# Optimization experiments

Measured on AMD Instinct MI355X. Metric: run time of the kernel, lower is better.

Reference implementation:

```python
import jax, jax.numpy as jnp
import numpy as np

K = 20
EPS = 1e-5

def _knn(x, k):
    # x: (B,C,N); returns indices of k nearest neighbors (incl. self): (B,N,k)
    xx = jnp.sum(x * x, axis=1)                          # (B,N)
    inner = jnp.einsum('bcn,bcm->bnm', x, x)             # (B,N,N)
    neg_d = 2.0 * inner - xx[:, :, None] - xx[:, None, :]
    return jax.lax.top_k(neg_d, k)[1]

def _graph_feature(x, k):
    # x: (B,C,N) -> (B,2C,N,k) with [x_j - x_i, x_i]
    idx = _knn(x, k)
    xt = jnp.transpose(x, (0, 2, 1))                     # (B,N,C)
    nb = jax.vmap(lambda f, i: f[i])(xt, idx)            # (B,N,k,C)
    ctr = xt[:, :, None, :]
    feat = jnp.concatenate([nb - ctr, jnp.broadcast_to(ctr, nb.shape)], axis=-1)
    return jnp.transpose(feat, (0, 3, 1, 2))

def _edge_block(h, w, g, b, k):
    # EdgeConv: graph feature -> 1x1 conv -> BN(eval, mean0/var1) -> LeakyReLU(0.2) -> max over k
    f = _graph_feature(h, k)
    f = jnp.einsum('oc,bcnk->bonk', w, f)
    f = g[None, :, None, None] * f / np.sqrt(1.0 + EPS) + b[None, :, None, None]
    f = jnp.where(f >= 0, f, 0.2 * f)
    return jnp.max(f, axis=-1)                           # (B,O,N)

def _forward(features_1, features_2, sw1, sg1, sb1, fw1, fg1, fb1, sw2, sg2, sb2, fw2, fg2, fb2, sw3, sg3, sb3, fw3, fg3, fb3, ew, eg, eb, att_w, tn_w, tn_wb, tn_bias, fc1_w, fc1_b, sc_w, sc_b):
    def dgcnn_pass(x):
        xyz = x[:, :3, :]
        sem = x[:, 3:, :]
        x1 = _edge_block(xyz, sw1, sg1, sb1, K)
        x2 = _edge_block(x1, sw2, sg2, sb2, K)
        x3 = _edge_block(x2, sw3, sg3, sb3, K)
        s1 = _edge_block(sem, fw1, fg1, fb1, K)
        s2 = _edge_block(s1, fw2, fg2, fb2, K)
        s3 = _edge_block(s2, fw3, fg3, fb3, K)
        h = jnp.concatenate([x3, s3], axis=1)            # (B,2*F3,N)
        h = jnp.einsum('oc,bcn->bon', ew, h)
        h = eg[None, :, None] * h / np.sqrt(1.0 + EPS) + eb[None, :, None]
        h = jnp.where(h >= 0, h, 0.2 * h)
        return jnp.transpose(h, (0, 2, 1))               # (B,N,F3)

    def attention(emb):
        gc = jnp.tanh(jnp.mean(jnp.einsum('bnf,fg->bng', emb, att_w), axis=1))  # (B,F)
        sc = jax.nn.sigmoid(jnp.einsum('bnf,bf->bn', emb, gc))[:, :, None]      # (B,N,1)
        pooled = jnp.einsum('bnf,bnk->bfk', emb, sc)                            # (B,F,1)
        return pooled, sc

    a1 = dgcnn_pass(features_1)
    a2 = dgcnn_pass(features_2)
    p1, att1 = attention(a1)
    p2, att2 = attention(a2)
    e1 = p1[:, :, 0]
    e2 = p2[:, :, 0]
    # NTN: e1^T W[:,:,t] e2 + V [e1;e2] + b
    scoring = jnp.einsum('bf,fgt,bg->bt', e1, tn_w, e2)
    block = jnp.einsum('tc,bc->bt', tn_wb, jnp.concatenate([e1, e2], axis=1))
    tscores = jax.nn.relu(scoring + block + tn_bias[:, 0][None, :])             # (B,T)
    h = jax.nn.relu(tscores @ fc1_w.T + fc1_b)
    score = jax.nn.sigmoid(h @ sc_w.T + sc_b).reshape(-1)                       # (B,)
    return score, att1, att2


def setup_inputs() -> dict:
    key = jax.random.key(0)
    ks = iter(jax.random.split(key, 40))
    def rn(shape, s=0.05):
        return jax.random.normal(next(ks), shape, dtype=jnp.float32) * s
    F1, F2, F3, T, BN = 64, 64, 128, 16, 16
    d = {}
    d['features_1'] = jax.random.normal(next(ks), (8, 131, 1024), dtype=jnp.float32)
    d['features_2'] = jax.random.normal(next(ks), (8, 131, 1024), dtype=jnp.float32)
    d['sw1'] = rn((F1, 6));        d['sg1'] = jnp.ones((F1,));  d['sb1'] = jnp.zeros((F1,))
    d['fw1'] = rn((F1, 256));      d['fg1'] = jnp.ones((F1,));  d['fb1'] = jnp.zeros((F1,))
    d['sw2'] = rn((F2, 2 * F1));   d['sg2'] = jnp.ones((F2,));  d['sb2'] = jnp.zeros((F2,))
    d['fw2'] = rn((F2, 2 * F1));   d['fg2'] = jnp.ones((F2,));  d['fb2'] = jnp.zeros((F2,))
    d['sw3'] = rn((F3, 2 * F2));   d['sg3'] = jnp.ones((F3,));  d['sb3'] = jnp.zeros((F3,))
    d['fw3'] = rn((F3, 2 * F2));   d['fg3'] = jnp.ones((F3,));  d['fb3'] = jnp.zeros((F3,))
    d['ew']  = rn((F3, 2 * F3));   d['eg']  = jnp.ones((F3,));  d['eb']  = jnp.zeros((F3,))
    d['att_w'] = rn((F3, F3))
    d['tn_w'] = rn((F3, F3, T))
    d['tn_wb'] = rn((T, 2 * F3))
    d['tn_bias'] = rn((T, 1))
    d['fc1_w'] = rn((BN, T));  d['fc1_b'] = jnp.zeros((BN,))
    d['sc_w'] = rn((1, BN));   d['sc_b'] = jnp.zeros((1,))
    return d


def reference(features_1, features_2, sw1, sg1, sb1, fw1, fg1, fb1, sw2, sg2, sb2, fw2, fg2, fb2, sw3, sg3, sb3, fw3, fg3, fb3, ew, eg, eb, att_w, tn_w, tn_wb, tn_bias, fc1_w, fc1_b, sc_w, sc_b):
    return _forward(features_1, features_2, sw1, sg1, sb1, fw1, fg1, fb1, sw2, sg2, sb2, fw2, fg2, fb2, sw3, sg3, sb3, fw3, fg3, fb3, ew, eg, eb, att_w, tn_w, tn_wb, tn_bias, fc1_w, fc1_b, sc_w, sc_b)
```

## Files before the change

kernel.cpp:

```cpp
#include <hip/hip_runtime.h>
#include <math.h>

#define INV_SQRT1P 0.99999500003749968754f

typedef short v8s  __attribute__((ext_vector_type(8)));
typedef float v16f __attribute__((ext_vector_type(16)));

static __device__ __forceinline__ float lrelu(float f){ return f >= 0.0f ? f : 0.2f*f; }

static __device__ __forceinline__ int lanecnt_below(unsigned long long m){
  int c = __builtin_amdgcn_mbcnt_lo((unsigned)m, 0u);
  return __builtin_amdgcn_mbcnt_hi((unsigned)(m >> 32), c);
}

__global__ void k_extract(const float* __restrict__ f, float* __restrict__ out, int c0, int Cout, int boff){
  int i = blockIdx.x*256 + threadIdx.x;
  int total = 8*Cout*1024;
  if (i >= total) return;
  int n  = i & 1023;
  int bc = i >> 10;
  int c  = bc % Cout;
  int b  = bc / Cout;
  out[((size_t)(((b+boff)<<10)+n))*Cout + c] = f[((size_t)(b*131 + c0 + c) << 10) + n];
}

__global__ __launch_bounds__(256) void k_pw(const float* __restrict__ X,
    unsigned short* __restrict__ PH, unsigned short* __restrict__ PL,
    float* __restrict__ xxout, const float* __restrict__ Wm,
    unsigned short* __restrict__ PWH, unsigned short* __restrict__ PWL,
    int C, int Kp, int O, int nwblk){
  int nkc = Kp >> 4;
  if ((int)blockIdx.x < nwblk){
    int gid = blockIdx.x*256 + threadIdx.x;
    int nchunk = (2*O/32)*nkc;
    if (gid >= nchunk*64) return;
    int lane = gid & 63;
    int chunk = gid >> 6;
    int jb = chunk / nkc, kc = chunk - jb*nkc;
    int j = jb*32 + (lane & 31);
    int k0 = kc*16 + ((lane>>5)<<3);
    unsigned short h[8], lo[8];
    #pragma unroll
    for (int t=0;t<8;t++){
      int k = k0 + t;
      float x = 0.f;
      if (k < C) x = (j < O) ? Wm[(size_t)j*2*C + k] : Wm[(size_t)(j-O)*2*C + C + k];
      unsigned u = __float_as_uint(x);
      unsigned h16 = (u + 0x7fffu + ((u>>16)&1u)) >> 16;
      float hf = __uint_as_float(h16 << 16);
      float lf = x - hf;
      unsigned ul = __float_as_uint(lf);
      unsigned l16 = (ul + 0x7fffu + ((ul>>16)&1u)) >> 16;
      h[t] = (unsigned short)h16; lo[t] = (unsigned short)l16;
    }
    size_t o = (size_t)chunk*512 + lane*8;
    *(v8s*)(PWH + o) = *(v8s*)h;
    *(v8s*)(PWL + o) = *(v8s*)lo;
  } else {
    int gid = (blockIdx.x - nwblk)*256 + threadIdx.x;
    int lane = gid & 63;
    int chunk = gid >> 6;
    int rb = chunk / nkc, kc = chunk - rb*nkc;
    int row = rb*32 + (lane & 31);
    int k0 = kc*16 + ((lane>>5)<<3);
    unsigned short h[8], lo[8];
    const float* Xr = X + (size_t)row*C;
    #pragma unroll
    for (int j=0;j<8;j++){
      int k = k0 + j;
      float x = (k < C) ? Xr[k] : 0.f;
      unsigned u = __float_as_uint(x);
      unsigned h16 = (u + 0x7fffu + ((u>>16)&1u)) >> 16;
      float hf = __uint_as_float(h16 << 16);
      float lf = x - hf;
      unsigned ul = __float_as_uint(lf);
      unsigned l16 = (ul + 0x7fffu + ((ul>>16)&1u)) >> 16;
      h[j] = (unsigned short)h16; lo[j] = (unsigned short)l16;
    }
    size_t o = (size_t)chunk*512 + lane*8;
    *(v8s*)(PH + o) = *(v8s*)h;
    *(v8s*)(PL + o) = *(v8s*)lo;
    if (kc == 0 && (lane & 32) == 0){
      float s = 0.f;
      for (int c=0;c<C;c++) s += Xr[c]*Xr[c];
      xxout[row] = s;
    }
  }
}

__global__ __launch_bounds__(512) void k_dy(const unsigned short* __restrict__ PH,
    const unsigned short* __restrict__ PL, const unsigned short* __restrict__ PWH,
    const unsigned short* __restrict__ PWL, const float* __restrict__ xx,
    int* __restrict__ idx, float* __restrict__ Y, int Kp, int N, int npair, int nymf){
  __shared__ float Sl[16][1024];
  int wave = threadIdx.x >> 6;
  int l = threadIdx.x & 63;
  int nkc = Kp >> 4;

  if ((int)blockIdx.x < nymf){
    int gw = blockIdx.x*8 + wave;
    int mt = gw / npair;
    int pair = gw - mt*npair;
    int jb0 = pair*2, jb1 = pair*2 + 1;
    size_t ao  = ((size_t)mt*nkc)*512 + l*8;
    size_t b0o = ((size_t)jb0*nkc)*512 + l*8;
    size_t b1o = ((size_t)jb1*nkc)*512 + l*8;
    v16f acc0, acc1;
    #pragma unroll
    for (int i=0;i<16;i++){ acc0[i] = 0.f; acc1[i] = 0.f; }
    for (int kc=0; kc<nkc; kc++){
      v8s Ah  = *(const v8s*)(PH + ao);
      v8s Al  = *(const v8s*)(PL + ao);
      v8s B0h = *(const v8s*)(PWH + b0o);
      v8s B0l = *(const v8s*)(PWL + b0o);
      v8s B1h = *(const v8s*)(PWH + b1o);
      v8s B1l = *(const v8s*)(PWL + b1o);
      acc0 = __builtin_amdgcn_mfma_f32_32x32x16_bf16(Ah, B0h, acc0, 0, 0, 0);
      acc1 = __builtin_amdgcn_mfma_f32_32x32x16_bf16(Ah, B1h, acc1, 0, 0, 0);
      acc0 = __builtin_amdgcn_mfma_f32_32x32x16_bf16(Ah, B0l, acc0, 0, 0, 0);
      acc1 = __builtin_amdgcn_mfma_f32_32x32x16_bf16(Ah, B1l, acc1, 0, 0, 0);
      acc0 = __builtin_amdgcn_mfma_f32_32x32x16_bf16(Al, B0h, acc0, 0, 0, 0);
      acc1 = __builtin_amdgcn_mfma_f32_32x32x16_bf16(Al, B1h, acc1, 0, 0, 0);
      ao += 512; b0o += 512; b1o += 512;
    }
    int rbase = mt*32;
    int c0 = pair*64 + (l & 31), c1 = c0 + 32;
    #pragma unroll
    for (int r=0;r<16;r++){
      int rl_ = (r&3) + ((r>>2)<<3) + ((l>>5)<<2);
      float* dst = Y + (size_t)(rbase + rl_)*N;
      dst[c0] = acc0[r];
      dst[c1] = acc1[r];
    }
    return;
  }

  int rb = blockIdx.x - nymf;
  int batch = rb >> 5;
  const float* xxb = xx + (batch<<10);
  int rbase_local = (rb & 31)*32;

  v16f acc[4];
  #pragma unroll
  for (int i=0;i<4;i++){
    #pragma unroll
    for (int j=0;j<16;j++) acc[i][j] = 0.f;
  }
  #pragma unroll
  for (int pp=0; pp<2; pp++){
    int pair = wave*2 + pp;
    size_t a   = ((size_t)rb*nkc)*512 + l*8;
    size_t b0o = ((size_t)(batch*32 + 2*pair)*nkc)*512 + l*8;
    size_t b1o = b0o + (size_t)nkc*512;
    for (int kc=0; kc<nkc; kc++){
      v8s Ah  = *(const v8s*)(PH + a);
      v8s Al  = *(const v8s*)(PL + a);
      v8s B0h = *(const v8s*)(PH + b0o);
      v8s B0l = *(const v8s*)(PL + b0o);
      v8s B1h = *(const v8s*)(PH + b1o);
      v8s B1l = *(const v8s*)(PL + b1o);
      acc[2*pp]   = __builtin_amdgcn_mfma_f32_32x32x16_bf16(Ah, B0h, acc[2*pp],   0, 0, 0);
      acc[2*pp+1] = __builtin_amdgcn_mfma_f32_32x32x16_bf16(Ah, B1h, acc[2*pp+1], 0, 0, 0);
      acc[2*pp]   = __builtin_amdgcn_mfma_f32_32x32x16_bf16(Ah, B0l, acc[2*pp],   0, 0, 0);
      acc[2*pp+1] = __builtin_amdgcn_mfma_f32_32x32x16_bf16(Ah, B1l, acc[2*pp+1], 0, 0, 0);
      acc[2*pp]   = __builtin_amdgcn_mfma_f32_32x32x16_bf16(Al, B0h, acc[2*pp],   0, 0, 0);
      acc[2*pp+1] = __builtin_amdgcn_mfma_f32_32x32x16_bf16(Al, B1h, acc[2*pp+1], 0, 0, 0);
      a += 512; b0o += 512; b1o += 512;
    }
  }

  #pragma unroll
  for (int h=0; h<2; h++){
    #pragma unroll
    for (int pp=0; pp<2; pp++){
      int pair = wave*2 + pp;
      int c0 = pair*64 + (l & 31), c1 = c0 + 32;
      float xc0 = xxb[c0], xc1 = xxb[c1];
      #pragma unroll
      for (int r = 0; r < 8; r++){
        int rr = h*8 + r;
        int rl = (rr&3) + (((rr>>2)&1)<<3) + ((l>>5)<<2);
        float xr = xxb[rbase_local + h*16 + rl];
        Sl[rl][c0] = 2.f*acc[2*pp][rr]   - xr - xc0;
        Sl[rl][c1] = 2.f*acc[2*pp+1][rr] - xr - xc1;
      }
    }
    __syncthreads();
    {
      int hi = l >> 5;
      int li = l & 31;
      int rloc = wave*2 + hi;
      int grow = rb*32 + h*16 + rloc;
      int out_base = grow*20;
      unsigned long long hm = hi ? 0xFFFFFFFF00000000ull : 0x00000000FFFFFFFFull;

      unsigned kv[32];
      #pragma unroll
      for (int j=0;j<32;j++){
        unsigned u = __float_as_uint(Sl[rloc][li + 32*j]);
        kv[j] = (u & 0x80000000u) ? ~u : (u | 0x80000000u);
      }

      unsigned lmax = kv[0];
      #pragma unroll
      for (int j=1;j<32;j++) lmax = lmax > kv[j] ? lmax : kv[j];

      unsigned tau = 0u;
      #pragma unroll
      for (int bit=31; bit>=0; --bit){
        unsigned cand = tau | (1u << bit);
        unsigned long long M = __ballot(lmax >= cand);
        int c = hi ? __popc((unsigned)(M >> 32)) : __popc((unsigned)M);
        tau = (c >= 20) ? cand : tau;
      }

      unsigned long long* sl = (unsigned long long*)&Sl[rloc][0];
      sl[li] = 0ull; sl[li+32] = 0ull;
      int b2 = 0;
      #pragma unroll
      for (int j=0;j<32;j++){
        bool p = kv[j] >= tau;
        unsigned long long M = __ballot(p) & hm;
        if (p){
          int s = b2 + lanecnt_below(M);
          if (s < 64) sl[s] = ((unsigned long long)kv[j] << 32) | (unsigned)(li + 32*j);
        }
        b2 += __popcll(M);
      }

      if (b2 <= 64){
        unsigned long long pk0 = sl[li], pk1 = sl[li+32];
        unsigned vcur = 0u;
        #pragma unroll
        for (int bit=31; bit>=0; --bit){
          unsigned long long cc = (unsigned long long)(vcur | (1u << bit)) << 32;
          unsigned long long B0 = __ballot(pk0 >= cc);
          unsigned long long B1 = __ballot(pk1 >= cc);
          int clo = __popc((unsigned)B0) + __popc((unsigned)B1);
          int chi = __popc((unsigned)(B0>>32)) + __popc((unsigned)(B1>>32));
          int c = hi ? chi : clo;
          vcur = (c >= 20) ? (vcur | (1u << bit)) : vcur;
        }
        unsigned k0 = (unsigned)(pk0 >> 32), k1 = (unsigned)(pk1 >> 32);
        unsigned long long G0 = __ballot(k0 > vcur) & hm;
        unsigned long long G1 = __ballot(k1 > vcur) & hm;
        int ng0 = __popcll(G0);
        int c1  = ng0 + __popcll(G1);
        if (k0 > vcur) idx[out_base + lanecnt_below(G0)] = (int)(pk0 & 0xffffffffu);
        if (k1 > vcur) idx[out_base + ng0 + lanecnt_below(G1)] = (int)(pk1 & 0xffffffffu);
        unsigned long long E0 = __ballot(k0 == vcur) & hm;
        unsigned long long E1 = __ballot(k1 == vcur) & hm;
        int ne0 = __popcll(E0);
        if (k0 == vcur){ int s = c1 + lanecnt_below(E0); if (s < 20) idx[out_base + s] = (int)(pk0 & 0xffffffffu); }
        if (k1 == vcur){ int s = c1 + ne0 + lanecnt_below(E1); if (s < 20) idx[out_base + s] = (int)(pk1 & 0xffffffffu); }
      } else {
        unsigned cur = 0u;
        #pragma unroll 1
        for (int bit=31; bit>=0; --bit){
          unsigned cand = cur | (1u << bit);
          int lc = 0;
          #pragma unroll
          for (int j=0;j<32;j++) lc += (kv[j] >= cand) ? 1 : 0;
          #pragma unroll
          for (int off=1; off<32; off<<=1) lc += __shfl_xor(lc, off, 64);
          cur = (lc >= 20) ? cand : cur;
        }
        int bse = 0;
        #pragma unroll 1
        for (int j=0;j<32;j++){
          unsigned long long Mg = __ballot(kv[j] > cur) & hm;
          if (kv[j] > cur){ int s = bse + lanecnt_below(Mg); idx[out_base + s] = li + 32*j; }
          bse += __popcll(Mg);
        }
        #pragma unroll 1
        for (int j=0;j<32;j++){
          unsigned long long Me = __ballot(kv[j] == cur) & hm;
          if (kv[j] == cur){ int s = bse + lanecnt_below(Me); if (s < 20) idx[out_base + s] = li + 32*j; }
          bse += __popcll(Me);
          if (bse >= 20) break;
        }
      }
    }
    __syncthreads();
  }
}

__global__ __launch_bounds__(256) void k_gthin(
    const float* __restrict__ Am, const float* __restrict__ Bm, float* __restrict__ Om,
    int K, int ldo, int wmode, const float* __restrict__ p1, const float* __restrict__ p2, int ep)
{
  __shared__ float As[64][33];
  __shared__ float Bs[64][68];
  int tid = threadIdx.x;
  int tx = tid & 15, ty = tid >> 4;
  int rbase = blockIdx.y*32, cbase = blockIdx.x*64;
  float acc[2][4];
  #pragma unroll
  for (int i=0;i<2;i++){ acc[i][0]=0.f; acc[i][1]=0.f; acc[i][2]=0.f; acc[i][3]=0.f; }

  for (int c0=0; c0<K; c0+=64){
    int cw = K - c0; if (cw > 64) cw = 64;
    #pragma unroll
    for (int p=0; p<2; p++){
      int idx = p*256 + tid;
      int kq = idx & 15, row = idx >> 4;
      const float* src = Am + (size_t)(rbase+row)*K + c0 + kq*4;
      float4 v = {0.f,0.f,0.f,0.f};
      if (kq*4 + 4 <= cw) v = *(const float4*)src;
      else {
        if (kq*4+0 < cw) v.x = src[0];
        if (kq*4+1 < cw) v.y = src[1];
        if (kq*4+2 < cw) v.z = src[2];
        if (kq*4+3 < cw) v.w = src[3];
      }
      As[kq*4+0][row]=v.x; As[kq*4+1][row]=v.y; As[kq*4+2][row]=v.z; As[kq*4+3][row]=v.w;
    }
    #pragma unroll
    for (int p=0; p<4; p++){
      int idx = p*256 + tid;
      int kq = idx & 15, col = idx >> 4;
      int j = cbase + col;
      const float* src = (wmode > 0)
          ? ((j < wmode) ? Bm + (size_t)j*2*K + c0 + kq*4
                         : Bm + (size_t)(j-wmode)*2*K + K + c0 + kq*4)
          : Bm + (size_t)j*K + c0 + kq*4;
      float4 v = {0.f,0.f,0.f,0.f};
      if (kq*4 + 4 <= cw) v = *(const float4*)src;
      else {
        if (kq*4+0 < cw) v.x = src[0];
        if (kq*4+1 < cw) v.y = src[1];
        if (kq*4+2 < cw) v.z = src[2];
        if (kq*4+3 < cw) v.w = src[3];
      }
      int swb = (kq & 14) << 1;
      int cs = col ^ swb;
      Bs[kq*4+0][cs]=v.x; Bs[kq*4+1][cs]=v.y; Bs[kq*4+2][cs]=v.z; Bs[kq*4+3][cs]=v.w;
    }
    __syncthreads();
    for (int k=0;k<cw;k++){
      int sw = ((k>>3)&7)<<2;
      float a0 = As[k][ty*2], a1 = As[k][ty*2+1];
      float b[4];
      *(float4*)b = *(const float4*)&Bs[k][(tx*4) ^ sw];
      acc[0][0]+=a0*b[0]; acc[0][1]+=a0*b[1]; acc[0][2]+=a0*b[2]; acc[0][3]+=a0*b[3];
      acc[1][0]+=a1*b[0]; acc[1][1]+=a1*b[1]; acc[1][2]+=a1*b[2]; acc[1][3]+=a1*b[3];
    }
    __syncthreads();
  }
  #pragma unroll
  for (int i=0;i<2;i++){
    int r = rbase + ty*2 + i;
    float o[4];
    #pragma unroll
    for (int j=0;j<4;j++){
      int cc = cbase + tx*4 + j;
      float v = acc[i][j];
      if (ep == 1) v = lrelu(p1[cc]*v*INV_SQRT1P + p2[cc]);
      o[j] = v;
    }
    *(float4*)(Om + (size_t)r*ldo + cbase + tx*4) = *(float4*)o;
  }
}

__global__ __launch_bounds__(256) void k_edge(const float* __restrict__ Y, const int* __restrict__ idx,
    const float* __restrict__ g, const float* __restrict__ bias,
    float* __restrict__ out, int O, int ldo, int ooff){
  int rpb = 256/O;
  int rloc = threadIdx.x/O;
  int o = threadIdx.x - rloc*O;
  int row = blockIdx.x*rpb + rloc;
  int b = row >> 10;
  __shared__ int js[4][20];
  int nj = rpb*20;
  if (threadIdx.x < nj) js[threadIdx.x/20][threadIdx.x%20] = idx[(blockIdx.x*rpb)*20 + threadIdx.x];
  __syncthreads();
  int O2 = O*2;
  float y1c = Y[(size_t)row*O2 + o];
  float d   = Y[(size_t)row*O2 + O + o] - y1c;
  float sc  = g[o] * INV_SQRT1P;
  float bb  = bias[o];
  const float* Yb = Y + ((size_t)(b<<10))*O2;
  float best = -1e38f;
  #pragma unroll
  for (int k=0;k<20;k++){
    float f = sc * (Yb[(size_t)js[rloc][k]*O2 + o] + d) + bb;
    best = fmaxf(best, lrelu(f));
  }
  out[(size_t)row*ldo + ooff + o] = best;
}

__global__ __launch_bounds__(1024) void k_meangc(const float* __restrict__ emb,
     const float* __restrict__ att_w, float* __restrict__ gc){
  int b = blockIdx.x; int f = threadIdx.x & 127; int ny = threadIdx.x >> 7;
  const float* e = emb + ((size_t)(b<<10) + ny*128)*128 + f;
  float s = 0.f;
  for (int n=0;n<128;n++) s += e[n*128];
  __shared__ float red[8][128];
  __shared__ float mr[128];
  red[ny][f] = s;
  __syncthreads();
  if (ny == 0){
    float t = 0.f;
    #pragma unroll
    for (int i=0;i<8;i++) t += red[i][f];
    mr[f] = t * (1.0f/1024.0f);
  }
  __syncthreads();
  if (threadIdx.x < 128){
    int g = threadIdx.x;
    float s2 = 0.f;
    for (int ff=0; ff<128; ff++) s2 += mr[ff]*att_w[ff*128+g];
    gc[b*128+g] = tanhf(s2);
  }
}

__global__ __launch_bounds__(64) void k_sc(const float* __restrict__ emb, const float* __restrict__ gc,
     float* __restrict__ sc, float* __restrict__ attout){
  int row = blockIdx.x; int l = threadIdx.x; int b = row >> 10;
  const float* e  = emb + (size_t)row*128;
  const float* gb = gc + b*128;
  float p = e[l]*gb[l] + e[l+64]*gb[l+64];
  #pragma unroll
  for (int off=32; off>0; off>>=1) p += __shfl_xor(p, off, 64);
  if (l == 0){
    float s = 1.0f/(1.0f + expf(-p));
    sc[row] = s;
    attout[row] = s;
  }
}

__global__ __launch_bounds__(1024) void k_pool(const float* __restrict__ emb, const float* __restrict__ sc,
     float* __restrict__ ep){
  int b = blockIdx.x; int f = threadIdx.x & 127; int ny = threadIdx.x >> 7;
  const float* e  = emb + ((size_t)(b<<10) + ny*128)*128 + f;
  const float* sb = sc + (b<<10) + ny*128;
  float s = 0.f;
  for (int n=0;n<128;n++) s += e[n*128]*sb[n];
  __shared__ float red[8][128];
  red[ny][f] = s;
  __syncthreads();
  if (ny == 0){
    float t = 0.f;
    #pragma unroll
    for (int i=0;i<8;i++) t += red[i][f];
    ep[b*128+f] = t;
  }
}

__global__ __launch_bounds__(256) void k_tnet(const float* __restrict__ e1, const float* __restrict__ e2,
    const float* __restrict__ tn_w, const float* __restrict__ tn_wb, const float* __restrict__ tn_bias,
    float* __restrict__ tsout){
  int b = blockIdx.x; int t = threadIdx.x; int tt = t & 15; int fs = t >> 4;
  __shared__ float E1[128], E2[128], red[16][17];
  if (t < 128){ E1[t] = e1[b*128+t]; E2[t] = e2[b*128+t]; }
  __syncthreads();
  float acc = 0.f;
  for (int f = fs*8; f < fs*8+8; f++){
    const float* tw = tn_w + f*128*16 + tt;
    float partial = 0.f;
    for (int g=0; g<128; g++) partial += E2[g]*tw[g*16];
    acc += E1[f]*partial;
  }
  red[fs][tt] = acc;
  __syncthreads();
  if (t < 16){
    float s = 0.f;
    #pragma unroll
    for (int i=0;i<16;i++) s += red[i][t];
    float acc2 = 0.f;
    for (int c=0;c<128;c++) acc2 += tn_wb[t*256+c]*E1[c] + tn_wb[t*256+128+c]*E2[c];
    float v = s + acc2 + tn_bias[t];
    tsout[b*16+t] = v > 0.f ? v : 0.f;
  }
}

__global__ __launch_bounds__(128) void k_score2(const float* __restrict__ ts,
   const float* __restrict__ fc1_w, const float* __restrict__ fc1_b,
   const float* __restrict__ sc_w, const float* __restrict__ sc_b, float* __restrict__ out){
  int t = threadIdx.x; int b = t >> 4, i = t & 15;
  __shared__ float h2[8][17];
  float a = 0.f;
  #pragma unroll
  for (int k=0;k<16;k++) a += ts[b*16+k]*fc1_w[i*16+k];
  a += fc1_b[i];
  h2[b][i] = a > 0.f ? a : 0.f;
  __syncthreads();
  if (t < 8){
    float s = 0.f;
    #pragma unroll
    for (int k=0;k<16;k++) s += h2[t][k]*sc_w[k];
    s += sc_b[0];
    out[t] = 1.0f/(1.0f + expf(-s));
  }
}

extern "C" void kernel_launch(void* const* d_in, const int* in_sizes, int n_in,
                              void* d_out, int out_size, void* d_ws, size_t ws_size,
                              hipStream_t stream){
  const float* f1  = (const float*)d_in[0];
  const float* f2  = (const float*)d_in[1];
  const float* sw1 = (const float*)d_in[2];  const float* sg1 = (const float*)d_in[3];  const float* sb1 = (const float*)d_in[4];
  const float* fw1 = (const float*)d_in[5];  const float* fg1 = (const float*)d_in[6];  const float* fb1 = (const float*)d_in[7];
  const float* sw2 = (const float*)d_in[8];  const float* sg2 = (const float*)d_in[9];  const float* sb2 = (const float*)d_in[10];
  const float* fw2 = (const float*)d_in[11]; const float* fg2 = (const float*)d_in[12]; const float* fb2 = (const float*)d_in[13];
  const float* sw3 = (const float*)d_in[14]; const float* sg3 = (const float*)d_in[15]; const float* sb3 = (const float*)d_in[16];
  const float* fw3 = (const float*)d_in[17]; const float* fg3 = (const float*)d_in[18]; const float* fb3 = (const float*)d_in[19];
  const float* ew  = (const float*)d_in[20]; const float* eg  = (const float*)d_in[21]; const float* eb  = (const float*)d_in[22];
  const float* att_w   = (const float*)d_in[23];
  const float* tn_w    = (const float*)d_in[24];
  const float* tn_wb   = (const float*)d_in[25];
  const float* tn_bias = (const float*)d_in[26];
  const float* fc1_w   = (const float*)d_in[27];
  const float* fc1_b   = (const float*)d_in[28];
  const float* sc_w    = (const float*)d_in[29];
  const float* sc_b    = (const float*)d_in[30];

  float* W    = (float*)d_ws;
  float* T0   = W;
  float* T1   = W + 2097152;
  float* X3S3 = W + 4194304;
  float* EMB  = W + 8388608;
  float* xx   = W + 10485760;
  float* gcb  = W + 10504192;
  float* scb  = W + 10506240;
  float* ep   = W + 10522624;
  float* tsb  = W + 10524672;
  int*   idxb = (int*)(W + 10524800);
  unsigned short* PH = (unsigned short*)(W + 10852480);
  unsigned short* PL = (unsigned short*)(W + 11901056);
  unsigned short* PWH = (unsigned short*)(W + 12949632);
  unsigned short* PWL = (unsigned short*)(W + 12966016);
  float* REG  = W + 12982400;

  (void)ws_size;
  float* out = (float*)d_out;

  auto edge = [&](const float* xin, int C, int O,
                  const float* w, const float* g, const float* bb,
                  float* xout, int ldo, int ooff){
    int Kp = (C + 15) & ~15;
    int nkc = Kp >> 4;
    int npair = 2*O/64;
    int nwblk = ((2*O/32)*nkc*64 + 255)/256;
    int nymf  = 64*npair;
    k_pw<<<nwblk + 128*nkc, 256, 0, stream>>>(xin, PH, PL, xx, w, PWH, PWL, C, Kp, O, nwblk);
    k_dy<<<nymf + 512, 512, 0, stream>>>(PH, PL, PWH, PWL, xx, idxb, REG, Kp, 2*O, npair, nymf);
    k_edge<<<16384/(256/O), 256, 0, stream>>>(REG, idxb, g, bb, xout, O, ldo, ooff);
  };

  k_extract<<<(8*3*1024+255)/256, 256, 0, stream>>>(f1, T0, 0, 3, 0);
  k_extract<<<(8*3*1024+255)/256, 256, 0, stream>>>(f2, T0, 0, 3, 8);
  edge(T0, 3,   64, sw1, sg1, sb1, T1, 64, 0);
  edge(T1, 64,  64, sw2, sg2, sb2, T0, 64, 0);
  edge(T0, 64, 128, sw3, sg3, sb3, X3S3, 256, 0);
  k_extract<<<(8*128*1024+255)/256, 256, 0, stream>>>(f1, T0, 3, 128, 0);
  k_extract<<<(8*128*1024+255)/256, 256, 0, stream>>>(f2, T0, 3, 128, 8);
  edge(T0, 128, 64, fw1, fg1, fb1, T1, 64, 0);
  edge(T1, 64,  64, fw2, fg2, fb2, T0, 64, 0);
  edge(T0, 64, 128, fw3, fg3, fb3, X3S3, 256, 128);
  k_gthin<<<dim3(2, 512, 1), 256, 0, stream>>>(X3S3, ew, EMB, 256, 128,
        0, eg, eb, 1);
  k_meangc<<<16, 1024, 0, stream>>>(EMB, att_w, gcb);
  k_sc<<<16384, 64, 0, stream>>>(EMB, gcb, scb, out + 8);
  k_pool<<<16, 1024, 0, stream>>>(EMB, scb, ep);

  k_tnet<<<8, 256, 0, stream>>>(ep, ep + 1024, tn_w, tn_wb, tn_bias, tsb);
  k_score2<<<1, 128, 0, stream>>>(tsb, fc1_w, fc1_b, sc_w, sc_b, out);
}
```

Baseline: 521.1 us.

## Merge extract launches, tile-transpose semantic extract, remap dy blocks, widen k_sc

Fuses the two xyz extraction launches into one kernel. Replaces the strided semantic-feature extraction with an LDS-tiled transpose so both reads and writes are coalesced. Remaps the k_dy row-block index so consecutive blocks fall in different batches, changing which blocks are co-resident and the cache locality. Packs four rows per block in k_sc to cut the block count.

```diff
diff --git a/kernel.cpp b/kernel.cpp
--- a/kernel.cpp
+++ b/kernel.cpp
@@ -13,15 +13,45 @@
   return __builtin_amdgcn_mbcnt_hi((unsigned)(m >> 32), c);
 }
 
-__global__ void k_extract(const float* __restrict__ f, float* __restrict__ out, int c0, int Cout, int boff){
+__global__ void k_ext3(const float* __restrict__ f1, const float* __restrict__ f2,
+                       float* __restrict__ out){
   int i = blockIdx.x*256 + threadIdx.x;
-  int total = 8*Cout*1024;
-  if (i >= total) return;
-  int n  = i & 1023;
-  int bc = i >> 10;
-  int c  = bc % Cout;
-  int b  = bc / Cout;
-  out[((size_t)(((b+boff)<<10)+n))*Cout + c] = f[((size_t)(b*131 + c0 + c) << 10) + n];
+  int half = 8*3*1024;
+  if (i >= 2*half) return;
+  const float* f = (i < half) ? f1 : f2;
+  int boff = (i < half) ? 0 : 8;
+  int ii = (i < half) ? i : i - half;
+  int n  = ii & 1023;
+  int bc = ii >> 10;
+  int c  = bc % 3;
+  int b  = bc / 3;
+  out[((size_t)(((b+boff)<<10)+n))*3 + c] = f[((size_t)(b*131 + c) << 10) + n];
+}
+
+__global__ __launch_bounds__(256) void k_extT(const float* __restrict__ f1,
+    const float* __restrict__ f2, float* __restrict__ out){
+  __shared__ float T[32][65];
+  int bid = blockIdx.x;
+  int nt = bid & 15;
+  int ct = (bid >> 4) & 3;
+  int bb = bid >> 6;
+  const float* f = (bb < 8) ? f1 : f2;
+  int b = bb & 7;
+  int tid = threadIdx.x;
+  #pragma unroll
+  for (int it=0; it<8; it++){
+    int cc = it*4 + (tid >> 6);
+    int nn = tid & 63;
+    T[cc][nn] = f[((size_t)(b*131 + 3 + ct*32 + cc) << 10) + nt*64 + nn];
+  }
+  __syncthreads();
+  size_t rowb = ((size_t)bb << 10) + nt*64;
+  #pragma unroll
+  for (int it=0; it<8; it++){
+    int nn = it*8 + (tid >> 5);
+    int c  = tid & 31;
+    out[(rowb + nn)*128 + ct*32 + c] = T[c][nn];
+  }
 }
 
 __global__ __launch_bounds__(256) void k_pw(const float* __restrict__ X,
@@ -135,7 +165,8 @@
     return;
   }
 
-  int rb = blockIdx.x - nymf;
+  int t = blockIdx.x - nymf;
+  int rb = ((t & 7) << 6) | (t >> 3);
   int batch = rb >> 5;
   const float* xxb = xx + (batch<<10);
   int rbase_local = (rb & 31)*32;
@@ -414,9 +445,12 @@
   }
 }
 
-__global__ __launch_bounds__(64) void k_sc(const float* __restrict__ emb, const float* __restrict__ gc,
+__global__ __launch_bounds__(256) void k_sc(const float* __restrict__ emb, const float* __restrict__ gc,
      float* __restrict__ sc, float* __restrict__ attout){
-  int row = blockIdx.x; int l = threadIdx.x; int b = row >> 10;
+  int wave = threadIdx.x >> 6;
+  int l = threadIdx.x & 63;
+  int row = blockIdx.x*4 + wave;
+  int b = row >> 10;
   const float* e  = emb + (size_t)row*128;
   const float* gb = gc + b*128;
   float p = e[l]*gb[l] + e[l+64]*gb[l+64];
@@ -548,20 +582,18 @@
     k_edge<<<16384/(256/O), 256, 0, stream>>>(REG, idxb, g, bb, xout, O, ldo, ooff);
   };
 
-  k_extract<<<(8*3*1024+255)/256, 256, 0, stream>>>(f1, T0, 0, 3, 0);
-  k_extract<<<(8*3*1024+255)/256, 256, 0, stream>>>(f2, T0, 0, 3, 8);
+  k_ext3<<<(2*8*3*1024+255)/256, 256, 0, stream>>>(f1, f2, T0);
   edge(T0, 3,   64, sw1, sg1, sb1, T1, 64, 0);
   edge(T1, 64,  64, sw2, sg2, sb2, T0, 64, 0);
   edge(T0, 64, 128, sw3, sg3, sb3, X3S3, 256, 0);
-  k_extract<<<(8*128*1024+255)/256, 256, 0, stream>>>(f1, T0, 3, 128, 0);
-  k_extract<<<(8*128*1024+255)/256, 256, 0, stream>>>(f2, T0, 3, 128, 8);
+  k_extT<<<1024, 256, 0, stream>>>(f1, f2, T0);
   edge(T0, 128, 64, fw1, fg1, fb1, T1, 64, 0);
   edge(T1, 64,  64, fw2, fg2, fb2, T0, 64, 0);
   edge(T0, 64, 128, fw3, fg3, fb3, X3S3, 256, 128);
   k_gthin<<<dim3(2, 512, 1), 256, 0, stream>>>(X3S3, ew, EMB, 256, 128,
         0, eg, eb, 1);
   k_meangc<<<16, 1024, 0, stream>>>(EMB, att_w, gcb);
-  k_sc<<<16384, 64, 0, stream>>>(EMB, gcb, scb, out + 8);
+  k_sc<<<4096, 256, 0, stream>>>(EMB, gcb, scb, out + 8);
   k_pool<<<16, 1024, 0, stream>>>(EMB, scb, ep);
 
   k_tnet<<<8, 256, 0, stream>>>(ep, ep + 1024, tn_w, tn_wb, tn_bias, tsb);
```

New measurement: 491.7 us. 5.7% less time.
